# Kernel optimization log

Hardware: AMD Instinct MI355X
Metric: run time of the kernel (lower is better)

## Reference

```python
import jax, jax.numpy as jnp
import numpy as np

HEAD_DIM = 128
N_HEADS = 16
N_KV_HEADS = 4
THETA = 10000.0
EPS = 1e-6


def setup_inputs() -> dict:
    key = jax.random.key(0)
    k1, k2, k3 = jax.random.split(key, 3)
    B, S = 2, 2048
    xq = jax.random.normal(k1, (B, S, N_HEADS * HEAD_DIM), dtype=jnp.float32)
    xk = jax.random.normal(k2, (B, S, N_KV_HEADS * HEAD_DIM), dtype=jnp.float32)
    xv = jax.random.normal(k3, (B, S, N_KV_HEADS * HEAD_DIM), dtype=jnp.float32)
    return {"xq": xq, "xk": xk, "xv": xv}


def _rope(x):
    # x: [b, h, s, d]; half-split rotary (y1 = x1*cos + x2*sin, y2 = -x1*sin + x2*cos)
    d = x.shape[-1]
    s = x.shape[2]
    inv_freq = (1.0 / THETA) ** (jnp.arange(0, d, 2, dtype=jnp.float32) / d)
    t = jnp.arange(s, dtype=jnp.float32)
    freqs = t[:, None] * inv_freq[None, :]          # [s, d/2]
    cos = jnp.cos(freqs)[None, None]                 # [1,1,s,d/2]
    sin = jnp.sin(freqs)[None, None]
    x1, x2 = jnp.split(x, 2, axis=-1)
    y1 = x1 * cos + x2 * sin
    y2 = -x1 * sin + x2 * cos
    return jnp.concatenate([y1, y2], axis=-1).astype(x.dtype)


def reference(xq, xk, xv):
    B, S, _ = xq.shape
    # b s (h a) -> b h s a
    q = xq.reshape(B, S, N_HEADS, HEAD_DIM).transpose(0, 2, 1, 3)
    k = xk.reshape(B, S, N_KV_HEADS, HEAD_DIM).transpose(0, 2, 1, 3)
    v = xv.reshape(B, S, N_KV_HEADS, HEAD_DIM).transpose(0, 2, 1, 3)
    # qk-norm (L2 normalize last dim with eps clamp, like F.normalize)
    q = q / jnp.maximum(jnp.linalg.norm(q, axis=-1, keepdims=True), EPS)
    k = k / jnp.maximum(jnp.linalg.norm(k, axis=-1, keepdims=True), EPS)
    # RoPE
    q = _rope(q)
    k = _rope(k)
    # GQA: repeat kv heads to match q heads
    rep = N_HEADS // N_KV_HEADS
    k = jnp.repeat(k, rep, axis=1)
    v = jnp.repeat(v, rep, axis=1)
    scale = 1.0 / jnp.sqrt(jnp.asarray(HEAD_DIM, dtype=q.dtype))
    scores = jnp.einsum('bhqd,bhkd->bhqk', q, k) * scale
    causal = jnp.tril(jnp.ones((S, S), dtype=bool))
    scores = jnp.where(causal[None, None], scores, jnp.asarray(-jnp.inf, scores.dtype))
    probs = jax.nn.softmax(scores, axis=-1)
    out = jnp.einsum('bhqk,bhkd->bhqd', probs, v)
    # b h s a -> b s (h a)
    return out.transpose(0, 2, 1, 3).reshape(B, S, N_HEADS * HEAD_DIM)
```

## Files before the change

### kernel.cpp

```cpp
#include <hip/hip_runtime.h>
#include <hip/hip_bf16.h>
#include <stdint.h>

#define S_LEN 2048
#define NB    2
#define HQ    16
#define HKV   4
#define HD    128
#define KVB   64
#define QBW   32
#define QBB   128

typedef __bf16 bf16_t;
typedef __attribute__((ext_vector_type(8)))  __bf16 bf16x8;
typedef __attribute__((ext_vector_type(4)))  float  f32x4;
typedef __attribute__((ext_vector_type(16))) float  f32x16;
typedef __attribute__((ext_vector_type(4)))  unsigned int u32x4;

__constant__ int kOrder24[24] = {7,22,23,20,21, 6,18,19,16,17, 5,14,15,12,13,
                                 4,10,11,8,9, 3, 2, 1, 0};

__device__ __forceinline__ void gload_lds16(const bf16_t* g, bf16_t* l) {
  __builtin_amdgcn_global_load_lds(
      (const __attribute__((address_space(1))) unsigned int*)g,
      (__attribute__((address_space(3))) unsigned int*)l, 16, 0, 0);
}
__device__ __forceinline__ uint32_t pack2(float lo, float hi) {
  uint32_t a = (uint32_t)__builtin_bit_cast(unsigned short, (bf16_t)lo);
  uint32_t b = (uint32_t)__builtin_bit_cast(unsigned short, (bf16_t)hi);
  return a | (b << 16);
}

__global__ void qk_preproc_kernel(const float* __restrict__ xq,
                                  const float* __restrict__ xk,
                                  bf16_t* __restrict__ Qr,
                                  bf16_t* __restrict__ Kf) {
  int wid  = (blockIdx.x * blockDim.x + threadIdx.x) >> 6;
  int lane = threadIdx.x & 63;
  const int per_bs = HQ + HKV;
  int b   = wid / (S_LEN * per_bs);
  int rem = wid - b * (S_LEN * per_bs);
  int s   = rem / per_bs;
  int hh  = rem - s * per_bs;
  const float* src;
  float scale;
  if (hh < HQ) {
    src = xq + ((size_t)(b * S_LEN + s) * (HQ * HD)) + hh * HD;
    scale = 0.08838834764831845f * 1.4426950408889634f;
  } else {
    src = xk + ((size_t)(b * S_LEN + s) * (HKV * HD)) + (hh - HQ) * HD;
    scale = 1.0f;
  }
  float x1 = src[lane];
  float x2 = src[64 + lane];
  float ss = x1 * x1 + x2 * x2;
  #pragma unroll
  for (int m = 1; m < 64; m <<= 1) ss += __shfl_xor(ss, m, 64);
  float rinv = scale / fmaxf(sqrtf(ss), 1e-6f);
  float inv = exp2f(-(float)lane * 0.20762050593046938f);
  float ang = (float)s * inv;
  float cs = cosf(ang), sn = sinf(ang);
  float q1 = x1 * rinv, q2 = x2 * rinv;
  bf16_t y1 = (bf16_t)(q1 * cs + q2 * sn);
  bf16_t y2 = (bf16_t)(q2 * cs - q1 * sn);
  if (hh < HQ) {
    bf16_t* dst = Qr + (((size_t)(b * HQ + hh) * S_LEN + s) * HD);
    dst[lane]      = y1;
    dst[64 + lane] = y2;
  } else {
    bf16_t* dst = Kf + ((size_t)((b * HKV + (hh - HQ)) * 32 + (s >> 6))) * (KVB * HD);
    const int sl = s & 63, half = sl >> 5, r0k = sl & 31;
    const int kk = lane >> 4, hi = (lane >> 3) & 1, pos = lane & 7;
    const int a1 = (kk * 128 + half * 64 + hi * 32 + r0k) * 8 + pos;
    dst[a1]        = y1;
    dst[a1 + 4096] = y2;
  }
}

__global__ void v_preproc_kernel(const float* __restrict__ xv,
                                 bf16_t* __restrict__ Vf) {
  __shared__ bf16_t tile[HD][66];
  int bh = blockIdx.x >> 5;
  int sc = blockIdx.x & 31;
  int b = bh >> 2, hh = bh & 3;
  const int d  = threadIdx.x & 127;
  const int s2 = threadIdx.x >> 7;
  const float* src = xv + (size_t)b * S_LEN * (HKV * HD) + hh * HD;
  #pragma unroll 4
  for (int it = 0; it < 32; ++it) {
    int sl = it * 2 + s2;
    int s  = sc * 64 + sl;
    tile[d][sl] = (bf16_t)src[(size_t)s * (HKV * HD) + d];
  }
  __syncthreads();
  bf16_t* dstb = Vf + ((size_t)bh * 32 + sc) * (HD * KVB);
  const int dd   = threadIdx.x >> 1;
  const int dt   = dd >> 5, r0v = dd & 31;
  const int cbase = (threadIdx.x & 1) * 4;
  #pragma unroll
  for (int i = 0; i < 4; ++i) {
    const int c = cbase + i;
    const int n = (c >> 1) * 256 + dt * 64 + (c & 1) * 32 + r0v;
    *reinterpret_cast<bf16x8*>(dstb + n * 8) =
        *reinterpret_cast<const bf16x8*>(&tile[dd][c * 8]);
  }
}

__global__ __launch_bounds__(256, 3)
void attn_kernel(const bf16_t* __restrict__ Qr,
                 const bf16_t* __restrict__ Kf,
                 const bf16_t* __restrict__ Vf,
                 float* __restrict__ out,
                 float* __restrict__ Opart,
                 float2* __restrict__ mlpart,
                 int split, int upb) {
  __shared__ bf16_t Kb[2][KVB * HD];
  __shared__ bf16_t Vb[HD * KVB];

  const int w    = threadIdx.x >> 6;
  const int lane = threadIdx.x & 63;
  const int r0   = lane & 31;
  const int hi   = lane >> 5;

  const int lid = (int)blockIdx.x;
  const int k   = (lid >> 3) % upb;
  const int bh  = (lid & 7) + 8 * ((lid >> 3) / upb);
  const int u   = split ? kOrder24[k] : (15 - k);
  int qt, t0, t1;
  if (!split || u < 8) {
    qt = u; t0 = 0; t1 = 2 * qt + 2;
  } else {
    int v = u - 8;
    qt = 8 + (v >> 1);
    int T = 2 * qt + 2, mid = qt + 1;
    if (v & 1) { t0 = mid; t1 = T; } else { t0 = 0; t1 = mid; }
  }
  const bool full = (t0 == 0) && (t1 == 2 * qt + 2);
  const int b    = bh >> 4;
  const int h    = bh & 15;
  const int kvh  = h >> 2;
  const int qw0  = qt * QBB + w * QBW;
  const int qrow = qw0 + r0;
  const int qmax = qw0 + 31;

  const bf16_t* Qbase = Qr + (size_t)(b * HQ  + h  ) * S_LEN * HD;
  const bf16_t* Kbase = Kf + (size_t)(b * HKV + kvh) * 32 * (KVB * HD);
  const bf16_t* Vbase = Vf + (size_t)(b * HKV + kvh) * 32 * (HD * KVB);

  const int soff = (w * 256 + lane) * 8;

  bf16x8 qf[8];
  #pragma unroll
  for (int kk = 0; kk < 8; ++kk)
    qf[kk] = *reinterpret_cast<const bf16x8*>(Qbase + (size_t)qrow * HD + kk * 16 + hi * 8);

  f32x16 accO[4];
  #pragma unroll
  for (int dt = 0; dt < 4; ++dt)
    #pragma unroll
    for (int e = 0; e < 16; ++e) accO[dt][e] = 0.f;
  float m = -3.0e38f, l = 0.f;

  {
    const bf16_t* kg = Kbase + (size_t)t0 * (KVB * HD);
    #pragma unroll
    for (int i = 0; i < 4; ++i)
      gload_lds16(kg + soff + i * 512, &Kb[0][soff + i * 512]);
  }

  for (int t = t0; t < t1; ++t) {
    const int pb = (t - t0) & 1;
    __builtin_amdgcn_s_barrier();
    {
      const bf16_t* vg = Vbase + (size_t)t * (HD * KVB);
      #pragma unroll
      for (int i = 0; i < 4; ++i)
        gload_lds16(vg + soff + i * 512, &Vb[soff + i * 512]);
      const int tn = (t + 1 < t1) ? t + 1 : t;
      const bf16_t* kg = Kbase + (size_t)tn * (KVB * HD);
      #pragma unroll
      for (int i = 0; i < 4; ++i)
        gload_lds16(kg + soff + i * 512, &Kb[pb ^ 1][soff + i * 512]);
    }
    asm volatile("s_waitcnt vmcnt(8)" ::: "memory");
    __builtin_amdgcn_sched_barrier(0);
    __builtin_amdgcn_s_barrier();
    __builtin_amdgcn_sched_barrier(0);

    const int kv0 = t * KVB;
    const bool active = (kv0 <= qmax);
    float p[32];
    u32x4 pw[4];
    if (active) {
      const bf16_t* kb = &Kb[pb][0];
      f32x16 st0, st1;
      #pragma unroll
      for (int e = 0; e < 16; ++e) { st0[e] = 0.f; st1[e] = 0.f; }
      __builtin_amdgcn_s_setprio(1);
      #pragma unroll
      for (int kk = 0; kk < 8; ++kk) {
        bf16x8 k0 = *reinterpret_cast<const bf16x8*>(kb + kk * 1024 + lane * 8);
        bf16x8 k1 = *reinterpret_cast<const bf16x8*>(kb + kk * 1024 + 512 + lane * 8);
        st0 = __builtin_amdgcn_mfma_f32_32x32x16_bf16(k0, qf[kk], st0, 0, 0, 0);
        st1 = __builtin_amdgcn_mfma_f32_32x32x16_bf16(k1, qf[kk], st1, 0, 0, 0);
      }
      __builtin_amdgcn_s_setprio(0);

      const bool need_mask = (kv0 + 63 > qw0);
      #pragma unroll
      for (int j = 0; j < 2; ++j)
        #pragma unroll
        for (int e = 0; e < 16; ++e) {
          float s = j ? st1[e] : st0[e];
          if (need_mask) {
            int kv = kv0 + j * 32 + (e & 3) + 8 * (e >> 2) + 4 * hi;
            s = (kv > qrow) ? -3.0e38f : s;
          }
          p[j * 16 + e] = s;
        }
      float mt[16];
      #pragma unroll
      for (int e = 0; e < 16; ++e) mt[e] = fmaxf(p[e], p[e + 16]);
      #pragma unroll
      for (int e = 0; e < 8; ++e) mt[e] = fmaxf(mt[e], mt[e + 8]);
      #pragma unroll
      for (int e = 0; e < 4; ++e) mt[e] = fmaxf(mt[e], mt[e + 4]);
      float lmx = fmaxf(fmaxf(mt[0], mt[1]), fmaxf(mt[2], mt[3]));
      float cmx = fmaxf(lmx, __shfl_xor(lmx, 32, 64));
      if (!__all(cmx <= m + 8.0f)) {
        float mnew = fmaxf(m, cmx);
        float resc = __builtin_amdgcn_exp2f(m - mnew);
        m = mnew;
        l *= resc;
        #pragma unroll
        for (int dt = 0; dt < 4; ++dt)
          #pragma unroll
          for (int e = 0; e < 16; ++e) accO[dt][e] *= resc;
      }
      #pragma unroll
      for (int e = 0; e < 32; ++e) p[e] = __builtin_amdgcn_exp2f(p[e] - m);
      float sv[16];
      #pragma unroll
      for (int e = 0; e < 16; ++e) sv[e] = p[e] + p[e + 16];
      #pragma unroll
      for (int e = 0; e < 8; ++e) sv[e] += sv[e + 8];
      #pragma unroll
      for (int e = 0; e < 4; ++e) sv[e] += sv[e + 4];
      float lsum = (sv[0] + sv[1]) + (sv[2] + sv[3]);
      l += lsum + __shfl_xor(lsum, 32, 64);

      #pragma unroll
      for (int j = 0; j < 2; ++j) {
        const int o = j * 16;
        {
          uint32_t A = pack2(p[o + 0], p[o + 1]);
          uint32_t C = pack2(p[o + 2], p[o + 3]);
          uint32_t B = pack2(p[o + 4], p[o + 5]);
          uint32_t D = pack2(p[o + 6], p[o + 7]);
          uint32_t At = __shfl_xor(A, 32, 64), Ct = __shfl_xor(C, 32, 64);
          uint32_t Bt = __shfl_xor(B, 32, 64), Dt = __shfl_xor(D, 32, 64);
          pw[2 * j] = hi ? (u32x4){Bt, Dt, B, D} : (u32x4){A, C, At, Ct};
        }
        {
          uint32_t A = pack2(p[o + 8],  p[o + 9]);
          uint32_t C = pack2(p[o + 10], p[o + 11]);
          uint32_t B = pack2(p[o + 12], p[o + 13]);
          uint32_t D = pack2(p[o + 14], p[o + 15]);
          uint32_t At = __shfl_xor(A, 32, 64), Ct = __shfl_xor(C, 32, 64);
          uint32_t Bt = __shfl_xor(B, 32, 64), Dt = __shfl_xor(D, 32, 64);
          pw[2 * j + 1] = hi ? (u32x4){Bt, Dt, B, D} : (u32x4){A, C, At, Ct};
        }
      }
    }

    asm volatile("s_waitcnt vmcnt(4)" ::: "memory");
    __builtin_amdgcn_sched_barrier(0);
    __builtin_amdgcn_s_barrier();
    __builtin_amdgcn_sched_barrier(0);

    if (active) {
      const bf16_t* vb = &Vb[0];
      __builtin_amdgcn_s_setprio(1);
      #pragma unroll
      for (int kk = 0; kk < 4; ++kk) {
        bf16x8 pf = __builtin_bit_cast(bf16x8, pw[kk]);
        #pragma unroll
        for (int dt = 0; dt < 4; ++dt) {
          bf16x8 vf = *reinterpret_cast<const bf16x8*>(vb + kk * 2048 + dt * 512 + lane * 8);
          accO[dt] = __builtin_amdgcn_mfma_f32_32x32x16_bf16(vf, pf, accO[dt], 0, 0, 0);
        }
      }
      __builtin_amdgcn_s_setprio(0);
    }
  }

  if (full) {
    const float inv = 1.0f / l;
    float* orow = out + ((size_t)(b * S_LEN + qrow) * (HQ * HD)) + h * HD + hi * 4;
    #pragma unroll
    for (int dt = 0; dt < 4; ++dt)
      #pragma unroll
      for (int rg = 0; rg < 4; ++rg) {
        f32x4 v4 = { accO[dt][4 * rg + 0] * inv, accO[dt][4 * rg + 1] * inv,
                     accO[dt][4 * rg + 2] * inv, accO[dt][4 * rg + 3] * inv };
        *reinterpret_cast<f32x4*>(orow + dt * 32 + rg * 8) = v4;
      }
  } else {
    const int c    = (t0 != 0) ? 1 : 0;
    const int pidx = ((bh << 3) + (qt - 8)) * 2 + c;
    float* Op = Opart + (size_t)pidx * (QBB * HD) + (size_t)(w * QBW + r0) * HD + hi * 4;
    #pragma unroll
    for (int dt = 0; dt < 4; ++dt)
      #pragma unroll
      for (int rg = 0; rg < 4; ++rg) {
        f32x4 v4 = { accO[dt][4 * rg + 0], accO[dt][4 * rg + 1],
                     accO[dt][4 * rg + 2], accO[dt][4 * rg + 3] };
        *reinterpret_cast<f32x4*>(Op + dt * 32 + rg * 8) = v4;
      }
    if (!hi) mlpart[(size_t)pidx * QBB + w * QBW + r0] = make_float2(m, l);
  }
}

__global__ void combine_kernel(const float* __restrict__ Opart,
                               const float2* __restrict__ mlpart,
                               float* __restrict__ out) {
  const int j  = blockIdx.x;
  const int bh = j >> 3;
  const int qt = 8 + (j & 7);
  const int b  = bh >> 4;
  const int h  = bh & 15;
  const int r  = threadIdx.x >> 1;
  const int d0 = (threadIdx.x & 1) * 64;
  const size_t p0 = (size_t)(j * 2)     * (QBB * HD) + (size_t)r * HD + d0;
  const size_t p1 = (size_t)(j * 2 + 1) * (QBB * HD) + (size_t)r * HD + d0;
  const float2 ml0 = mlpart[(size_t)(j * 2)     * QBB + r];
  const float2 ml1 = mlpart[(size_t)(j * 2 + 1) * QBB + r];
  const float M  = fmaxf(ml0.x, ml1.x);
  float a0 = exp2f(ml0.x - M), a1 = exp2f(ml1.x - M);
  const float inv = 1.0f / (a0 * ml0.y + a1 * ml1.y);
  a0 *= inv; a1 *= inv;
  const int qrow = qt * QBB + r;
  float* orow = out + ((size_t)(b * S_LEN + qrow) * (HQ * HD)) + h * HD + d0;
  #pragma unroll
  for (int i = 0; i < 16; ++i) {
    f32x4 o0 = *reinterpret_cast<const f32x4*>(Opart + p0 + i * 4);
    f32x4 o1 = *reinterpret_cast<const f32x4*>(Opart + p1 + i * 4);
    f32x4 res = { a0 * o0[0] + a1 * o1[0], a0 * o0[1] + a1 * o1[1],
                  a0 * o0[2] + a1 * o1[2], a0 * o0[3] + a1 * o1[3] };
    *reinterpret_cast<f32x4*>(orow + i * 4) = res;
  }
}

extern "C" void kernel_launch(void* const* d_in, const int* in_sizes, int n_in,
                              void* d_out, int out_size, void* d_ws, size_t ws_size,
                              hipStream_t stream) {
  const float* xq = (const float*)d_in[0];
  const float* xk = (const float*)d_in[1];
  const float* xv = (const float*)d_in[2];
  float* out = (float*)d_out;

  char* ws = (char*)d_ws;
  size_t off = 0;
  bf16_t* Qr = (bf16_t*)(ws + off); off += (size_t)NB * HQ  * S_LEN * HD * sizeof(bf16_t);
  bf16_t* Kf = (bf16_t*)(ws + off); off += (size_t)NB * HKV * S_LEN * HD * sizeof(bf16_t);
  bf16_t* Vf = (bf16_t*)(ws + off); off += (size_t)NB * HKV * S_LEN * HD * sizeof(bf16_t);
  float*  Opart  = (float*)(ws + off);  off += (size_t)512 * QBB * HD * sizeof(float);
  float2* mlpart = (float2*)(ws + off); off += (size_t)512 * QBB * sizeof(float2);
  const int split = (ws_size >= off) ? 1 : 0;
  const int upb   = split ? 24 : 16;

  const int nrow = NB * S_LEN * (HQ + HKV);
  qk_preproc_kernel<<<nrow / 4, 256, 0, stream>>>(xq, xk, Qr, Kf);

  v_preproc_kernel<<<NB * HKV * 32, 256, 0, stream>>>(xv, Vf);

  attn_kernel<<<32 * upb, 256, 0, stream>>>(Qr, Kf, Vf, out, Opart, mlpart,
                                            split, upb);
  if (split)
    combine_kernel<<<256, 256, 0, stream>>>(Opart, mlpart, out);
}
```

Measured before the change: 109.1 us.

## Single-buffer K in LDS to raise attention occupancy; split V preproc blocks

Removes the K double buffer. The next K tile is now loaded into the single buffer after QK^T finishes, behind an extra barrier, which cuts LDS per block to 32KB so launch bounds can rise from 3 to 4 blocks per CU. The V preprocessing kernel is also split into twice as many blocks, each handling half a 64-row chunk, to give it more parallelism. The trade-off is less overlap of K loads with compute and one more barrier per iteration, in exchange for more resident waves.

```diff
diff --git a/kernel.cpp b/kernel.cpp
--- a/kernel.cpp
+++ b/kernel.cpp
@@ -79,34 +79,37 @@
 
 __global__ void v_preproc_kernel(const float* __restrict__ xv,
                                  bf16_t* __restrict__ Vf) {
-  __shared__ bf16_t tile[HD][66];
-  int bh = blockIdx.x >> 5;
-  int sc = blockIdx.x & 31;
-  int b = bh >> 2, hh = bh & 3;
+  __shared__ bf16_t tile[HD][34];
+  const int bid = blockIdx.x;
+  const int bh  = bid >> 6;
+  const int r6  = bid & 63;
+  const int sc  = r6 >> 1;
+  const int j   = r6 & 1;
+  const int b = bh >> 2, hh = bh & 3;
   const int d  = threadIdx.x & 127;
   const int s2 = threadIdx.x >> 7;
   const float* src = xv + (size_t)b * S_LEN * (HKV * HD) + hh * HD;
   #pragma unroll 4
-  for (int it = 0; it < 32; ++it) {
+  for (int it = 0; it < 16; ++it) {
     int sl = it * 2 + s2;
-    int s  = sc * 64 + sl;
+    int s  = sc * 64 + j * 32 + sl;
     tile[d][sl] = (bf16_t)src[(size_t)s * (HKV * HD) + d];
   }
   __syncthreads();
   bf16_t* dstb = Vf + ((size_t)bh * 32 + sc) * (HD * KVB);
   const int dd   = threadIdx.x >> 1;
   const int dt   = dd >> 5, r0v = dd & 31;
-  const int cbase = (threadIdx.x & 1) * 4;
-  #pragma unroll
-  for (int i = 0; i < 4; ++i) {
-    const int c = cbase + i;
-    const int n = (c >> 1) * 256 + dt * 64 + (c & 1) * 32 + r0v;
+  #pragma unroll
+  for (int i = 0; i < 2; ++i) {
+    const int cl = (threadIdx.x & 1) * 2 + i;
+    const int c  = j * 4 + cl;
+    const int n  = (c >> 1) * 256 + dt * 64 + (c & 1) * 32 + r0v;
     *reinterpret_cast<bf16x8*>(dstb + n * 8) =
-        *reinterpret_cast<const bf16x8*>(&tile[dd][c * 8]);
-  }
-}
-
-__global__ __launch_bounds__(256, 3)
+        *reinterpret_cast<const bf16x8*>(&tile[dd][cl * 8]);
+  }
+}
+
+__global__ __launch_bounds__(256, 4)
 void attn_kernel(const bf16_t* __restrict__ Qr,
                  const bf16_t* __restrict__ Kf,
                  const bf16_t* __restrict__ Vf,
@@ -114,7 +117,7 @@
                  float* __restrict__ Opart,
                  float2* __restrict__ mlpart,
                  int split, int upb) {
-  __shared__ bf16_t Kb[2][KVB * HD];
+  __shared__ bf16_t Kb[KVB * HD];
   __shared__ bf16_t Vb[HD * KVB];
 
   const int w    = threadIdx.x >> 6;
@@ -165,24 +168,18 @@
     const bf16_t* kg = Kbase + (size_t)t0 * (KVB * HD);
     #pragma unroll
     for (int i = 0; i < 4; ++i)
-      gload_lds16(kg + soff + i * 512, &Kb[0][soff + i * 512]);
+      gload_lds16(kg + soff + i * 512, &Kb[soff + i * 512]);
   }
 
   for (int t = t0; t < t1; ++t) {
-    const int pb = (t - t0) & 1;
     __builtin_amdgcn_s_barrier();
     {
       const bf16_t* vg = Vbase + (size_t)t * (HD * KVB);
       #pragma unroll
       for (int i = 0; i < 4; ++i)
         gload_lds16(vg + soff + i * 512, &Vb[soff + i * 512]);
-      const int tn = (t + 1 < t1) ? t + 1 : t;
-      const bf16_t* kg = Kbase + (size_t)tn * (KVB * HD);
-      #pragma unroll
-      for (int i = 0; i < 4; ++i)
-        gload_lds16(kg + soff + i * 512, &Kb[pb ^ 1][soff + i * 512]);
-    }
-    asm volatile("s_waitcnt vmcnt(8)" ::: "memory");
+    }
+    asm volatile("s_waitcnt vmcnt(4)" ::: "memory");
     __builtin_amdgcn_sched_barrier(0);
     __builtin_amdgcn_s_barrier();
     __builtin_amdgcn_sched_barrier(0);
@@ -192,15 +189,14 @@
     float p[32];
     u32x4 pw[4];
     if (active) {
-      const bf16_t* kb = &Kb[pb][0];
       f32x16 st0, st1;
       #pragma unroll
       for (int e = 0; e < 16; ++e) { st0[e] = 0.f; st1[e] = 0.f; }
       __builtin_amdgcn_s_setprio(1);
       #pragma unroll
       for (int kk = 0; kk < 8; ++kk) {
-        bf16x8 k0 = *reinterpret_cast<const bf16x8*>(kb + kk * 1024 + lane * 8);
-        bf16x8 k1 = *reinterpret_cast<const bf16x8*>(kb + kk * 1024 + 512 + lane * 8);
+        bf16x8 k0 = *reinterpret_cast<const bf16x8*>(&Kb[kk * 1024 + lane * 8]);
+        bf16x8 k1 = *reinterpret_cast<const bf16x8*>(&Kb[kk * 1024 + 512 + lane * 8]);
         st0 = __builtin_amdgcn_mfma_f32_32x32x16_bf16(k0, qf[kk], st0, 0, 0, 0);
         st1 = __builtin_amdgcn_mfma_f32_32x32x16_bf16(k1, qf[kk], st1, 0, 0, 0);
       }
@@ -218,6 +214,18 @@
           }
           p[j * 16 + e] = s;
         }
+    }
+
+    __builtin_amdgcn_s_barrier();
+    {
+      const int tn = (t + 1 < t1) ? t + 1 : t;
+      const bf16_t* kg = Kbase + (size_t)tn * (KVB * HD);
+      #pragma unroll
+      for (int i = 0; i < 4; ++i)
+        gload_lds16(kg + soff + i * 512, &Kb[soff + i * 512]);
+    }
+
+    if (active) {
       float mt[16];
       #pragma unroll
       for (int e = 0; e < 16; ++e) mt[e] = fmaxf(p[e], p[e + 16]);
@@ -279,14 +287,13 @@
     __builtin_amdgcn_sched_barrier(0);
 
     if (active) {
-      const bf16_t* vb = &Vb[0];
       __builtin_amdgcn_s_setprio(1);
       #pragma unroll
       for (int kk = 0; kk < 4; ++kk) {
         bf16x8 pf = __builtin_bit_cast(bf16x8, pw[kk]);
         #pragma unroll
         for (int dt = 0; dt < 4; ++dt) {
-          bf16x8 vf = *reinterpret_cast<const bf16x8*>(vb + kk * 2048 + dt * 512 + lane * 8);
+          bf16x8 vf = *reinterpret_cast<const bf16x8*>(&Vb[kk * 2048 + dt * 512 + lane * 8]);
           accO[dt] = __builtin_amdgcn_mfma_f32_32x32x16_bf16(vf, pf, accO[dt], 0, 0, 0);
         }
       }
@@ -372,7 +379,7 @@
   const int nrow = NB * S_LEN * (HQ + HKV);
   qk_preproc_kernel<<<nrow / 4, 256, 0, stream>>>(xq, xk, Qr, Kf);
 
-  v_preproc_kernel<<<NB * HKV * 32, 256, 0, stream>>>(xv, Vf);
+  v_preproc_kernel<<<NB * HKV * 64, 256, 0, stream>>>(xv, Vf);
 
   attn_kernel<<<32 * upb, 256, 0, stream>>>(Qr, Kf, Vf, out, Opart, mlpart,
                                             split, upb);
```

After: 227.8 us. +108.8%, slower.
